# Kernel tuning notes

Measured on AMD Instinct MI355X. Metric: run time of the kernel, lower is better.

Reference implementation:

```python
import jax, jax.numpy as jnp
import numpy as np

B, T, D, U = 64, 2048, 512, 512

def setup_inputs() -> dict:
    key = jax.random.key(0)
    ks = jax.random.split(key, 5)
    scale = 1.0 / np.sqrt(D)
    return {
        "features": jax.random.normal(ks[0], (B, T, D), dtype=jnp.float32),
        "hidden": jax.random.normal(ks[1], (B, D), dtype=jnp.float32),
        "W1": jax.random.normal(ks[2], (D, U), dtype=jnp.float32) * scale,
        "b1": jnp.zeros((U,), dtype=jnp.float32),
        "W2": jax.random.normal(ks[3], (D, U), dtype=jnp.float32) * scale,
        "b2": jnp.zeros((U,), dtype=jnp.float32),
        "V": jax.random.normal(ks[4], (U, 1), dtype=jnp.float32) * (1.0 / np.sqrt(U)),
        "bV": jnp.zeros((1,), dtype=jnp.float32),
    }

def reference(features, hidden, W1, b1, W2, b2, V, bV):
    # features: [B, T, D]; hidden: [B, D]
    proj_f = jnp.einsum('btd,du->btu', features, W1) + b1          # [B, T, U]
    proj_h = (hidden @ W2 + b2)[:, None, :]                        # [B, 1, U]
    score = jnp.tanh(proj_f + proj_h) @ V + bV                     # [B, T, 1]
    attention_weights = jax.nn.softmax(score, axis=1)              # [B, T, 1]
    context_vector = jnp.sum(attention_weights * features, axis=1) # [B, D]
    return (context_vector, attention_weights)
```

## Files before the change

### kernel.cpp

```cpp
#include <hip/hip_runtime.h>
#include <hip/hip_bf16.h>

#define BB 64
#define TT 2048
#define DD 512
#define UU 512
#define MM (BB * TT)
#define CTX_ELEMS (BB * DD)
#define ATTN_OFF  CTX_ELEMS

typedef __bf16 bf16x8 __attribute__((ext_vector_type(8)));
typedef float  f32x4  __attribute__((ext_vector_type(4)));
typedef unsigned short u16x8 __attribute__((ext_vector_type(8)));
typedef unsigned int u32;

#define GLOBAL_AS __attribute__((address_space(1)))
#define LDS_AS    __attribute__((address_space(3)))

__device__ __forceinline__ unsigned short f2bf(float f) {
    union { float f; unsigned u; } x; x.f = f;
    unsigned r = x.u + 0x7fffu + ((x.u >> 16) & 1u);
    return (unsigned short)(r >> 16);
}

__device__ __forceinline__ float tanh_fast(float x) {
    x = fminf(fmaxf(x, -10.f), 10.f);
    float e = __builtin_amdgcn_exp2f(x * 2.885390082f);
    return (e - 1.0f) * __builtin_amdgcn_rcpf(e + 1.0f);
}

__global__ void k_w1t(const float* __restrict__ W1, unsigned short* __restrict__ W1T) {
    int gid = blockIdx.x * 256 + threadIdx.x;
    int u  = gid & 511;
    int dc = gid >> 9;
    int d0 = dc * 8;
    u16x8 pk;
    #pragma unroll
    for (int e = 0; e < 8; ++e)
        pk[e] = f2bf(W1[(size_t)(d0 + e) * UU + u]);
    int nt = u >> 7, n = u & 127;
    int kt = dc >> 2, kc = dc & 3;
    size_t off = ((size_t)(nt * 16 + kt) * 8192 + kc * 2048 + n * 16) / 2;
    *(u16x8*)(W1T + off) = pk;
}

__global__ void k_phc(const float* __restrict__ hidden, const float* __restrict__ W2,
                      const float* __restrict__ b1, const float* __restrict__ b2,
                      float* __restrict__ phc) {
    const int b = blockIdx.x;
    const int u = threadIdx.x;
    const float* h = hidden + (size_t)b * DD;
    float acc = b1[u] + b2[u];
    #pragma unroll 8
    for (int d = 0; d < DD; ++d)
        acc += h[d] * W2[(size_t)d * UU + u];
    phc[(size_t)b * UU + u] = acc;
}

__launch_bounds__(256, 3)
__global__ void k_score(const float* __restrict__ feat,
                        const unsigned short* __restrict__ W1T,
                        const float* __restrict__ phc,
                        const float* __restrict__ V,
                        float* __restrict__ part) {
    __shared__ float sA[128 * 32];
    __shared__ unsigned short sB[4096];
    __shared__ float sRed[4][64];

    const int tid  = threadIdx.x;
    const int lane = tid & 63;
    const int w    = tid >> 6;
    const int wr   = w >> 1, wc = w & 1;

    const int rb  = blockIdx.x;
    const int xcd = rb & 7;
    const int uu  = rb >> 3;
    const int gy  = uu & 3;
    const int gx  = xcd * 128 + (uu >> 2);
    const int m0  = gx * 128;
    const int b   = m0 >> 11;

    f32x4 acc[4][4];
    #pragma unroll
    for (int i = 0; i < 4; ++i)
        #pragma unroll
        for (int j = 0; j < 4; ++j)
            acc[i][j] = (f32x4){0.f, 0.f, 0.f, 0.f};

    const char* fbase0 = (const char*)feat + (size_t)m0 * 2048;
    const char* bslab0 = (const char*)W1T + (size_t)gy * 16 * 8192;

    for (int kt = 0; kt < 16; ++kt) {
        const char* bslab = bslab0 + kt * 8192;
        #pragma unroll
        for (int p = 0; p < 2; ++p) {
            int s = p * 256 + tid;
            const char* src = bslab + s * 16;
            char* dst = (char*)sB + (size_t)(p * 256 + (tid & ~63)) * 16;
            __builtin_amdgcn_global_load_lds((const GLOBAL_AS u32*)src, (LDS_AS u32*)dst, 16, 0, 0);
        }
        const char* fbase = fbase0 + kt * 128;
        #pragma unroll
        for (int j = 0; j < 4; ++j) {
            int s = j * 256 + tid;
            int row = s >> 3;
            int cpos = s & 7;
            int c = cpos ^ (row & 7);
            const char* src = fbase + (size_t)row * 2048 + c * 16;
            char* dst = (char*)sA + (size_t)(j * 256 + (tid & ~63)) * 16;
            __builtin_amdgcn_global_load_lds((const GLOBAL_AS u32*)src, (LDS_AS u32*)dst, 16, 0, 0);
        }
        __syncthreads();

        const int kc = lane >> 4;
        bf16x8 bfr[4];
        #pragma unroll
        for (int ns = 0; ns < 4; ++ns) {
            int n = wc * 64 + ns * 16 + (lane & 15);
            bfr[ns] = *(const bf16x8*)((const char*)sB + kc * 2048 + n * 16);
        }
        #pragma unroll
        for (int ms = 0; ms < 4; ++ms) {
            int m = wr * 64 + ms * 16 + (lane & 15);
            int c0 = (2 * kc) ^ (m & 7);
            int c1 = (2 * kc + 1) ^ (m & 7);
            f32x4 a0 = *(const f32x4*)((const char*)sA + m * 128 + c0 * 16);
            f32x4 a1 = *(const f32x4*)((const char*)sA + m * 128 + c1 * 16);
            bf16x8 af;
            #pragma unroll
            for (int j = 0; j < 4; ++j) { af[j] = (__bf16)a0[j]; af[4 + j] = (__bf16)a1[j]; }
            #pragma unroll
            for (int ns = 0; ns < 4; ++ns)
                acc[ms][ns] = __builtin_amdgcn_mfma_f32_16x16x32_bf16(af, bfr[ns], acc[ms][ns], 0, 0, 0);
        }
        __syncthreads();
    }

    float pc[4], vv[4];
    #pragma unroll
    for (int ns = 0; ns < 4; ++ns) {
        int ug = gy * 128 + wc * 64 + ns * 16 + (lane & 15);
        pc[ns] = phc[(size_t)b * UU + ug];
        vv[ns] = V[ug];
    }
    float pr[4][4];
    #pragma unroll
    for (int ms = 0; ms < 4; ++ms)
        #pragma unroll
        for (int rg = 0; rg < 4; ++rg) {
            float s = 0.f;
            #pragma unroll
            for (int ns = 0; ns < 4; ++ns)
                s += tanh_fast(acc[ms][ns][rg] + pc[ns]) * vv[ns];
            pr[ms][rg] = s;
        }
    #pragma unroll
    for (int off = 1; off < 16; off <<= 1)
        #pragma unroll
        for (int ms = 0; ms < 4; ++ms)
            #pragma unroll
            for (int rg = 0; rg < 4; ++rg)
                pr[ms][rg] += __shfl_xor(pr[ms][rg], off, 64);
    if ((lane & 15) == 0) {
        int rowg = lane >> 4;
        #pragma unroll
        for (int ms = 0; ms < 4; ++ms)
            #pragma unroll
            for (int rg = 0; rg < 4; ++rg)
                sRed[w][ms * 16 + rowg * 4 + rg] = pr[ms][rg];
    }
    __syncthreads();
    if (tid < 128) {
        int wrx = tid >> 6, ml = tid & 63;
        float v = sRed[2 * wrx][ml] + sRed[2 * wrx + 1][ml];
        part[(size_t)gy * MM + m0 + tid] = v;
    }
}

__global__ void k_softmax(const float* __restrict__ part, float* __restrict__ dout) {
    const int b = blockIdx.x, tid = threadIdx.x;
    float* sc = dout + ATTN_OFF + (size_t)b * TT;
    float v[8];
    float mx = -3.4e38f;
    #pragma unroll
    for (int i = 0; i < 8; ++i) {
        int t = tid + 256 * i;
        size_t idx = (size_t)b * TT + t;
        v[i] = part[idx] + part[MM + idx] + part[2 * MM + idx] + part[3 * MM + idx];
        mx = fmaxf(mx, v[i]);
    }
    __shared__ float red[256];
    red[tid] = mx; __syncthreads();
    for (int s = 128; s >= 1; s >>= 1) {
        if (tid < s) red[tid] = fmaxf(red[tid], red[tid + s]);
        __syncthreads();
    }
    mx = red[0]; __syncthreads();
    float sum = 0.f;
    #pragma unroll
    for (int i = 0; i < 8; ++i) { v[i] = __expf(v[i] - mx); sum += v[i]; }
    red[tid] = sum; __syncthreads();
    for (int s = 128; s >= 1; s >>= 1) {
        if (tid < s) red[tid] += red[tid + s];
        __syncthreads();
    }
    float inv = 1.0f / red[0];
    #pragma unroll
    for (int i = 0; i < 8; ++i) sc[tid + 256 * i] = v[i] * inv;
}

__global__ void k_context(const float* __restrict__ feat, float* __restrict__ dout) {
    const int b = blockIdx.x, dc = blockIdx.y;
    const int dq = threadIdx.x & 15;
    const int ty = threadIdx.x >> 4;
    const int d = dc * 64 + dq * 4;
    const float* wgt = dout + ATTN_OFF + (size_t)b * TT;
    const float* f = feat + (size_t)b * TT * DD + d;
    float4 acc = {0.f, 0.f, 0.f, 0.f};
    #pragma unroll 4
    for (int i = 0; i < TT / 16; ++i) {
        int t = i * 16 + ty;
        float wv = wgt[t];
        float4 fv = *(const float4*)(f + (size_t)t * DD);
        acc.x += wv * fv.x; acc.y += wv * fv.y;
        acc.z += wv * fv.z; acc.w += wv * fv.w;
    }
    __shared__ float4 red[16][16];
    red[ty][dq] = acc; __syncthreads();
    if (ty == 0) {
        float4 s = red[0][dq];
        #pragma unroll
        for (int k = 1; k < 16; ++k) {
            float4 r = red[k][dq];
            s.x += r.x; s.y += r.y; s.z += r.z; s.w += r.w;
        }
        *(float4*)(dout + (size_t)b * DD + d) = s;
    }
}

extern "C" void kernel_launch(void* const* d_in, const int* in_sizes, int n_in,
                              void* d_out, int out_size, void* d_ws, size_t ws_size,
                              hipStream_t stream) {
    (void)in_sizes; (void)n_in; (void)out_size; (void)ws_size;
    const float* feat   = (const float*)d_in[0];
    const float* hidden = (const float*)d_in[1];
    const float* W1     = (const float*)d_in[2];
    const float* b1     = (const float*)d_in[3];
    const float* W2     = (const float*)d_in[4];
    const float* b2     = (const float*)d_in[5];
    const float* V      = (const float*)d_in[6];

    unsigned short* W1T = (unsigned short*)d_ws;
    float* phc  = (float*)((char*)d_ws + 512 * 1024);
    float* part = (float*)((char*)d_ws + 640 * 1024);
    float* out  = (float*)d_out;

    hipLaunchKernelGGL(k_w1t,     dim3(128),    dim3(256), 0, stream, W1, W1T);
    hipLaunchKernelGGL(k_phc,     dim3(64),     dim3(512), 0, stream, hidden, W2, b1, b2, phc);
    hipLaunchKernelGGL(k_score,   dim3(4096),   dim3(256), 0, stream, feat, W1T, phc, V, part);
    hipLaunchKernelGGL(k_softmax, dim3(64),     dim3(256), 0, stream, part, out);
    hipLaunchKernelGGL(k_context, dim3(64, 8),  dim3(256), 0, stream, feat, out);
}
```

Measured before the change: 196.0 us.

## Double-buffer score GEMM with register-staged bf16 A tiles and larger blocks

Rewrites the score GEMM kernel to use 512-thread blocks that each cover 256 rows, with a K tile of 64 and double-buffered LDS for both operands. The next tile's feature loads and W1 loads are issued while the current tile's MFMAs run. Features are converted to bf16 once in registers before being written to LDS, instead of being stored as fp32 and converted by every wave on read. This is meant to hide global-memory latency and halve LDS traffic for A. The cost is higher register and LDS use per block and hand-written waitcnt/barrier scheduling that is fragile.

```diff
diff --git a/kernel.cpp b/kernel.cpp
--- a/kernel.cpp
+++ b/kernel.cpp
@@ -38,9 +38,9 @@
     #pragma unroll
     for (int e = 0; e < 8; ++e)
         pk[e] = f2bf(W1[(size_t)(d0 + e) * UU + u]);
-    int nt = u >> 7, n = u & 127;
-    int kt = dc >> 2, kc = dc & 3;
-    size_t off = ((size_t)(nt * 16 + kt) * 8192 + kc * 2048 + n * 16) / 2;
+    int gy = u >> 7, n = u & 127;
+    int kt = dc >> 3, kc = dc & 7;
+    size_t off = (((size_t)(gy * 8 + kt) * 8 + kc) * 1024 + n * 8);
     *(u16x8*)(W1T + off) = pk;
 }
 
@@ -57,29 +57,45 @@
     phc[(size_t)b * UU + u] = acc;
 }
 
-__launch_bounds__(256, 3)
+__launch_bounds__(512, 1)
 __global__ void k_score(const float* __restrict__ feat,
                         const unsigned short* __restrict__ W1T,
                         const float* __restrict__ phc,
                         const float* __restrict__ V,
                         float* __restrict__ part) {
-    __shared__ float sA[128 * 32];
-    __shared__ unsigned short sB[4096];
-    __shared__ float sRed[4][64];
+    __shared__ __align__(16) unsigned short sA[2 * 8 * 256 * 8];
+    __shared__ __align__(16) unsigned short sB[2 * 8 * 128 * 8];
+    __shared__ float sRed[8][64];
 
     const int tid  = threadIdx.x;
     const int lane = tid & 63;
     const int w    = tid >> 6;
-    const int wr   = w >> 1, wc = w & 1;
-
-    const int rb  = blockIdx.x;
-    const int xcd = rb & 7;
-    const int uu  = rb >> 3;
-    const int gy  = uu & 3;
-    const int gx  = xcd * 128 + (uu >> 2);
-    const int m0  = gx * 128;
+    const int wm   = w >> 1, wc = w & 1;
+
+    const int bid = blockIdx.x;
+    const int xcd = bid & 7;
+    const int idx = bid >> 3;
+    const int gy  = idx & 3;
+    const int mt  = xcd * 64 + (idx >> 2);
+    const int m0  = mt * 256;
     const int b   = m0 >> 11;
 
+    const int kcl   = lane >> 4;
+    const int rlane = lane & 15;
+
+    const char* fsrc = (const char*)feat +
+        (((size_t)(m0 + (tid >> 3)) * 512) + (size_t)(tid & 7) * 8) * 4;
+    const char* bsl = (const char*)W1T + (size_t)gy * 8 * 16384;
+
+    float pc[4], vv[4];
+    #pragma unroll
+    for (int ns = 0; ns < 4; ++ns) {
+        int ug = gy * 128 + wc * 64 + ns * 16 + rlane;
+        pc[ns] = phc[(size_t)b * UU + ug];
+        vv[ns] = V[ug];
+    }
+
+    f32x4 rA[8];
     f32x4 acc[4][4];
     #pragma unroll
     for (int i = 0; i < 4; ++i)
@@ -87,62 +103,92 @@
         for (int j = 0; j < 4; ++j)
             acc[i][j] = (f32x4){0.f, 0.f, 0.f, 0.f};
 
-    const char* fbase0 = (const char*)feat + (size_t)m0 * 2048;
-    const char* bslab0 = (const char*)W1T + (size_t)gy * 16 * 8192;
-
-    for (int kt = 0; kt < 16; ++kt) {
-        const char* bslab = bslab0 + kt * 8192;
-        #pragma unroll
-        for (int p = 0; p < 2; ++p) {
-            int s = p * 256 + tid;
-            const char* src = bslab + s * 16;
-            char* dst = (char*)sB + (size_t)(p * 256 + (tid & ~63)) * 16;
-            __builtin_amdgcn_global_load_lds((const GLOBAL_AS u32*)src, (LDS_AS u32*)dst, 16, 0, 0);
-        }
-        const char* fbase = fbase0 + kt * 128;
-        #pragma unroll
-        for (int j = 0; j < 4; ++j) {
-            int s = j * 256 + tid;
-            int row = s >> 3;
-            int cpos = s & 7;
-            int c = cpos ^ (row & 7);
-            const char* src = fbase + (size_t)row * 2048 + c * 16;
-            char* dst = (char*)sA + (size_t)(j * 256 + (tid & ~63)) * 16;
-            __builtin_amdgcn_global_load_lds((const GLOBAL_AS u32*)src, (LDS_AS u32*)dst, 16, 0, 0);
-        }
-        __syncthreads();
-
-        const int kc = lane >> 4;
-        bf16x8 bfr[4];
-        #pragma unroll
-        for (int ns = 0; ns < 4; ++ns) {
-            int n = wc * 64 + ns * 16 + (lane & 15);
-            bfr[ns] = *(const bf16x8*)((const char*)sB + kc * 2048 + n * 16);
-        }
-        #pragma unroll
-        for (int ms = 0; ms < 4; ++ms) {
-            int m = wr * 64 + ms * 16 + (lane & 15);
-            int c0 = (2 * kc) ^ (m & 7);
-            int c1 = (2 * kc + 1) ^ (m & 7);
-            f32x4 a0 = *(const f32x4*)((const char*)sA + m * 128 + c0 * 16);
-            f32x4 a1 = *(const f32x4*)((const char*)sA + m * 128 + c1 * 16);
-            bf16x8 af;
-            #pragma unroll
-            for (int j = 0; j < 4; ++j) { af[j] = (__bf16)a0[j]; af[4 + j] = (__bf16)a1[j]; }
-            #pragma unroll
-            for (int ns = 0; ns < 4; ++ns)
-                acc[ms][ns] = __builtin_amdgcn_mfma_f32_16x16x32_bf16(af, bfr[ns], acc[ms][ns], 0, 0, 0);
-        }
-        __syncthreads();
-    }
-
-    float pc[4], vv[4];
-    #pragma unroll
-    for (int ns = 0; ns < 4; ++ns) {
-        int ug = gy * 128 + wc * 64 + ns * 16 + (lane & 15);
-        pc[ns] = phc[(size_t)b * UU + ug];
-        vv[ns] = V[ug];
-    }
+#define VMW(N)  asm volatile("s_waitcnt vmcnt(" #N ")" ::: "memory")
+#define LGKM0() asm volatile("s_waitcnt lgkmcnt(0)" ::: "memory")
+
+#define ISSUE_A(tt_, p_) do {                                                    \
+    rA[4*(p_)+0] = *(const f32x4*)(fsrc + (size_t)(2*(p_))  *131072 + (tt_)*256);     \
+    rA[4*(p_)+1] = *(const f32x4*)(fsrc + (size_t)(2*(p_))  *131072 + (tt_)*256 + 16);\
+    rA[4*(p_)+2] = *(const f32x4*)(fsrc + (size_t)(2*(p_)+1)*131072 + (tt_)*256);     \
+    rA[4*(p_)+3] = *(const f32x4*)(fsrc + (size_t)(2*(p_)+1)*131072 + (tt_)*256 + 16);\
+    } while (0)
+
+#define ISSUE_B(tt_, p_) do {                                                    \
+    const char* src_ = bsl + (size_t)(tt_) * 16384 + (p_) * 8192 + tid * 16;     \
+    char* dst_ = (char*)sB + ((tt_) & 1) * 16384 + (p_) * 8192 + (tid & ~63) * 16;\
+    __builtin_amdgcn_global_load_lds((const GLOBAL_AS u32*)src_,                 \
+                                     (LDS_AS u32*)dst_, 16, 0, 0); } while (0)
+
+#define WRITE_A(tt_) do {                                                        \
+    const int kcw_ = tid & 7;                                                    \
+    _Pragma("unroll")                                                            \
+    for (int j_ = 0; j_ < 4; ++j_) {                                             \
+        bf16x8 q_;                                                               \
+        _Pragma("unroll")                                                        \
+        for (int e_ = 0; e_ < 4; ++e_) {                                         \
+            q_[e_]     = (__bf16)rA[2*j_][e_];                                   \
+            q_[4 + e_] = (__bf16)rA[2*j_ + 1][e_];                               \
+        }                                                                        \
+        int row_ = j_ * 64 + (tid >> 3);                                         \
+        int byt_ = ((tt_) & 1) * 32768 + kcw_ * 4096 + ((row_ * 16) ^ (kcw_ * 16));\
+        *(bf16x8*)((char*)sA + byt_) = q_;                                       \
+    } } while (0)
+
+#define PH(t_, p_, PRE_, VM_) do {                                               \
+    bf16x8 af[4], bfr[4];                                                        \
+    _Pragma("unroll")                                                            \
+    for (int ms_ = 0; ms_ < 4; ++ms_) {                                          \
+        int kc_ = (p_) * 4 + kcl;                                                \
+        int row_ = wm * 64 + ms_ * 16 + rlane;                                   \
+        af[ms_] = *(const bf16x8*)((const char*)sA + ((t_) & 1) * 32768 +        \
+                   kc_ * 4096 + ((row_ * 16) ^ (kc_ * 16)));                     \
+    }                                                                            \
+    _Pragma("unroll")                                                            \
+    for (int ns_ = 0; ns_ < 4; ++ns_) {                                          \
+        int kc_ = (p_) * 4 + kcl;                                                \
+        bfr[ns_] = *(const bf16x8*)((const char*)sB + ((t_) & 1) * 16384 +       \
+                    kc_ * 2048 + (wc * 64 + ns_ * 16 + rlane) * 16);             \
+    }                                                                            \
+    if (PRE_) { ISSUE_A((t_) + 1, p_); ISSUE_B((t_) + 1, p_); }                  \
+    if ((VM_) == 0) VMW(5); else if ((VM_) == 1) VMW(1); else if ((VM_) == 2) VMW(0); \
+    if ((p_) == 1 && (PRE_)) WRITE_A((t_) + 1);                                  \
+    LGKM0();                                                                     \
+    __builtin_amdgcn_s_barrier();                                                \
+    __builtin_amdgcn_sched_barrier(0);                                           \
+    __builtin_amdgcn_s_setprio(1);                                               \
+    _Pragma("unroll")                                                            \
+    for (int ms_ = 0; ms_ < 4; ++ms_)                                            \
+        _Pragma("unroll")                                                        \
+        for (int ns_ = 0; ns_ < 4; ++ns_)                                        \
+            acc[ms_][ns_] = __builtin_amdgcn_mfma_f32_16x16x32_bf16(             \
+                af[ms_], bfr[ns_], acc[ms_][ns_], 0, 0, 0);                      \
+    __builtin_amdgcn_s_setprio(0); } while (0)
+
+    ISSUE_A(0, 0);
+    ISSUE_A(0, 1);
+    ISSUE_B(0, 0);
+    ISSUE_B(0, 1);
+    VMW(1);
+    WRITE_A(0);
+    LGKM0();
+    __builtin_amdgcn_s_barrier();
+
+    PH(0, 0, 1, 0); PH(0, 1, 1, 1);
+    PH(1, 0, 1, 0); PH(1, 1, 1, 1);
+    PH(2, 0, 1, 0); PH(2, 1, 1, 1);
+    PH(3, 0, 1, 0); PH(3, 1, 1, 1);
+    PH(4, 0, 1, 0); PH(4, 1, 1, 1);
+    PH(5, 0, 1, 0); PH(5, 1, 1, 1);
+    PH(6, 0, 1, 0); PH(6, 1, 1, 1);
+    PH(7, 0, 0, 2); PH(7, 1, 0, 3);
+
+#undef PH
+#undef WRITE_A
+#undef ISSUE_B
+#undef ISSUE_A
+#undef VMW
+#undef LGKM0
+
     float pr[4][4];
     #pragma unroll
     for (int ms = 0; ms < 4; ++ms)
@@ -161,6 +207,7 @@
             #pragma unroll
             for (int rg = 0; rg < 4; ++rg)
                 pr[ms][rg] += __shfl_xor(pr[ms][rg], off, 64);
+    __syncthreads();
     if ((lane & 15) == 0) {
         int rowg = lane >> 4;
         #pragma unroll
@@ -170,9 +217,9 @@
                 sRed[w][ms * 16 + rowg * 4 + rg] = pr[ms][rg];
     }
     __syncthreads();
-    if (tid < 128) {
-        int wrx = tid >> 6, ml = tid & 63;
-        float v = sRed[2 * wrx][ml] + sRed[2 * wrx + 1][ml];
+    if (tid < 256) {
+        int wmx = tid >> 6, r = tid & 63;
+        float v = sRed[2 * wmx][r] + sRed[2 * wmx + 1][r];
         part[(size_t)gy * MM + m0 + tid] = v;
     }
 }
@@ -257,7 +304,7 @@
 
     hipLaunchKernelGGL(k_w1t,     dim3(128),    dim3(256), 0, stream, W1, W1T);
     hipLaunchKernelGGL(k_phc,     dim3(64),     dim3(512), 0, stream, hidden, W2, b1, b2, phc);
-    hipLaunchKernelGGL(k_score,   dim3(4096),   dim3(256), 0, stream, feat, W1T, phc, V, part);
+    hipLaunchKernelGGL(k_score,   dim3(2048),   dim3(512), 0, stream, feat, W1T, phc, V, part);
     hipLaunchKernelGGL(k_softmax, dim3(64),     dim3(256), 0, stream, part, out);
     hipLaunchKernelGGL(k_context, dim3(64, 8),  dim3(256), 0, stream, feat, out);
 }
```

Result: slower. 225.9 us (+15.3%).

## Pipeline score GEMM with register-staged bf16 A tile and double-buffered B

Applied to the files above, without the earlier changes.

The score kernel's main loop now uses K-steps of 64 instead of 32 (8 iterations). The next feature tile is prefetched into registers and the next W1 tile goes into a second LDS buffer while MFMAs run on the current one. Features are converted to bf16 once when stored to LDS, with an XOR swizzle, instead of being re-converted from fp32 LDS by each wave. The W1 pre-transpose layout changes to match. This aims to hide global-load latency and cut LDS traffic and conversion work, at the cost of more registers and hand-placed waitcnt/barrier ordering that could limit occupancy or be fragile.

```diff
diff --git a/kernel.cpp b/kernel.cpp
--- a/kernel.cpp
+++ b/kernel.cpp
@@ -38,10 +38,11 @@
     #pragma unroll
     for (int e = 0; e < 8; ++e)
         pk[e] = f2bf(W1[(size_t)(d0 + e) * UU + u]);
-    int nt = u >> 7, n = u & 127;
-    int kt = dc >> 2, kc = dc & 3;
-    size_t off = ((size_t)(nt * 16 + kt) * 8192 + kc * 2048 + n * 16) / 2;
-    *(u16x8*)(W1T + off) = pk;
+    int gy = u >> 7, n = u & 127;
+    int kt = dc >> 3, kc8 = dc & 7;
+    size_t off = (size_t)gy * 131072 + (size_t)kt * 16384 + kc8 * 2048
+               + ((n * 16) ^ (kc8 << 4));
+    *(u16x8*)((char*)W1T + off) = pk;
 }
 
 __global__ void k_phc(const float* __restrict__ hidden, const float* __restrict__ W2,
@@ -63,14 +64,15 @@
                         const float* __restrict__ phc,
                         const float* __restrict__ V,
                         float* __restrict__ part) {
-    __shared__ float sA[128 * 32];
-    __shared__ unsigned short sB[4096];
+    __shared__ __align__(16) unsigned short sA[8 * 128 * 8];
+    __shared__ __align__(16) unsigned short sB[2][8 * 128 * 8];
     __shared__ float sRed[4][64];
 
-    const int tid  = threadIdx.x;
-    const int lane = tid & 63;
-    const int w    = tid >> 6;
-    const int wr   = w >> 1, wc = w & 1;
+    const int tid   = threadIdx.x;
+    const int lane  = tid & 63;
+    const int w     = tid >> 6;
+    const int wm    = w >> 1, wc = w & 1;
+    const int rlane = lane & 15;
 
     const int rb  = blockIdx.x;
     const int xcd = rb & 7;
@@ -80,6 +82,22 @@
     const int m0  = gx * 128;
     const int b   = m0 >> 11;
 
+    const char* bsl = (const char*)W1T + (size_t)gy * 131072;
+
+    const int row_s = tid >> 1;
+    const int h_s   = tid & 1;
+    const char* fA = (const char*)feat +
+        ((size_t)(m0 + row_s) * 512 + (size_t)h_s * 32) * 4;
+
+    float pc[4], vv[4];
+    #pragma unroll
+    for (int ns = 0; ns < 4; ++ns) {
+        int ug = gy * 128 + wc * 64 + ns * 16 + rlane;
+        pc[ns] = phc[(size_t)b * UU + ug];
+        vv[ns] = V[ug];
+    }
+
+    f32x4 rS[8];
     f32x4 acc[4][4];
     #pragma unroll
     for (int i = 0; i < 4; ++i)
@@ -87,62 +105,85 @@
         for (int j = 0; j < 4; ++j)
             acc[i][j] = (f32x4){0.f, 0.f, 0.f, 0.f};
 
-    const char* fbase0 = (const char*)feat + (size_t)m0 * 2048;
-    const char* bslab0 = (const char*)W1T + (size_t)gy * 16 * 8192;
-
-    for (int kt = 0; kt < 16; ++kt) {
-        const char* bslab = bslab0 + kt * 8192;
-        #pragma unroll
-        for (int p = 0; p < 2; ++p) {
-            int s = p * 256 + tid;
-            const char* src = bslab + s * 16;
-            char* dst = (char*)sB + (size_t)(p * 256 + (tid & ~63)) * 16;
-            __builtin_amdgcn_global_load_lds((const GLOBAL_AS u32*)src, (LDS_AS u32*)dst, 16, 0, 0);
-        }
-        const char* fbase = fbase0 + kt * 128;
-        #pragma unroll
-        for (int j = 0; j < 4; ++j) {
-            int s = j * 256 + tid;
-            int row = s >> 3;
-            int cpos = s & 7;
-            int c = cpos ^ (row & 7);
-            const char* src = fbase + (size_t)row * 2048 + c * 16;
-            char* dst = (char*)sA + (size_t)(j * 256 + (tid & ~63)) * 16;
-            __builtin_amdgcn_global_load_lds((const GLOBAL_AS u32*)src, (LDS_AS u32*)dst, 16, 0, 0);
-        }
-        __syncthreads();
-
-        const int kc = lane >> 4;
-        bf16x8 bfr[4];
-        #pragma unroll
-        for (int ns = 0; ns < 4; ++ns) {
-            int n = wc * 64 + ns * 16 + (lane & 15);
-            bfr[ns] = *(const bf16x8*)((const char*)sB + kc * 2048 + n * 16);
-        }
-        #pragma unroll
-        for (int ms = 0; ms < 4; ++ms) {
-            int m = wr * 64 + ms * 16 + (lane & 15);
-            int c0 = (2 * kc) ^ (m & 7);
-            int c1 = (2 * kc + 1) ^ (m & 7);
-            f32x4 a0 = *(const f32x4*)((const char*)sA + m * 128 + c0 * 16);
-            f32x4 a1 = *(const f32x4*)((const char*)sA + m * 128 + c1 * 16);
-            bf16x8 af;
-            #pragma unroll
-            for (int j = 0; j < 4; ++j) { af[j] = (__bf16)a0[j]; af[4 + j] = (__bf16)a1[j]; }
-            #pragma unroll
-            for (int ns = 0; ns < 4; ++ns)
-                acc[ms][ns] = __builtin_amdgcn_mfma_f32_16x16x32_bf16(af, bfr[ns], acc[ms][ns], 0, 0, 0);
-        }
-        __syncthreads();
-    }
-
-    float pc[4], vv[4];
-    #pragma unroll
-    for (int ns = 0; ns < 4; ++ns) {
-        int ug = gy * 128 + wc * 64 + ns * 16 + (lane & 15);
-        pc[ns] = phc[(size_t)b * UU + ug];
-        vv[ns] = V[ug];
-    }
+#define ISSUE_A(kt_) do {                                                     \
+    _Pragma("unroll")                                                         \
+    for (int q_ = 0; q_ < 8; ++q_)                                            \
+        rS[q_] = *(const f32x4*)(fA + (kt_) * 256 + q_ * 16); } while (0)
+
+#define ISSUE_B(kt_) do {                                                     \
+    _Pragma("unroll")                                                         \
+    for (int p_ = 0; p_ < 4; ++p_) {                                          \
+        const char* src_ = bsl + (size_t)(kt_) * 16384 + p_ * 4096 + tid * 16;\
+        char* dst_ = (char*)&sB[(kt_) & 1][0] + p_ * 4096 + (tid & ~63) * 16; \
+        __builtin_amdgcn_global_load_lds((const GLOBAL_AS u32*)src_,          \
+                                         (LDS_AS u32*)dst_, 16, 0, 0);        \
+    } } while (0)
+
+#define WRITE_A() do {                                                        \
+    _Pragma("unroll")                                                         \
+    for (int j_ = 0; j_ < 4; ++j_) {                                          \
+        bf16x8 q_;                                                            \
+        _Pragma("unroll")                                                     \
+        for (int e_ = 0; e_ < 4; ++e_) {                                      \
+            q_[e_]     = (__bf16)rS[2 * j_][e_];                              \
+            q_[4 + e_] = (__bf16)rS[2 * j_ + 1][e_];                          \
+        }                                                                     \
+        int kc8_ = 4 * h_s + j_;                                              \
+        *(bf16x8*)((char*)sA + kc8_ * 2048 + ((row_s * 16) ^ (kc8_ << 4))) = q_; \
+    } } while (0)
+
+#define DO_C(c_, cb_) do {                                                    \
+    const int kc8_ = (c_) * 4 + (lane >> 4);                                  \
+    const int xr_  = kc8_ << 4;                                               \
+    bf16x8 af_[4], bf_[4];                                                    \
+    _Pragma("unroll")                                                         \
+    for (int ms_ = 0; ms_ < 4; ++ms_)                                         \
+        af_[ms_] = *(const bf16x8*)((const char*)sA + kc8_ * 2048 +           \
+                   (((wm * 64 + ms_ * 16 + rlane) * 16) ^ xr_));              \
+    _Pragma("unroll")                                                         \
+    for (int ns_ = 0; ns_ < 4; ++ns_)                                         \
+        bf_[ns_] = *(const bf16x8*)((const char*)&sB[cb_][0] + kc8_ * 2048 +  \
+                   (((wc * 64 + ns_ * 16 + rlane) * 16) ^ xr_));              \
+    _Pragma("unroll")                                                         \
+    for (int ms_ = 0; ms_ < 4; ++ms_)                                         \
+        _Pragma("unroll")                                                     \
+        for (int ns_ = 0; ns_ < 4; ++ns_)                                     \
+            acc[ms_][ns_] = __builtin_amdgcn_mfma_f32_16x16x32_bf16(          \
+                af_[ms_], bf_[ns_], acc[ms_][ns_], 0, 0, 0); } while (0)
+
+#define STEP(kt_) do {                                                        \
+    if ((kt_) < 7) {                                                          \
+        ISSUE_A((kt_) + 1); ISSUE_B((kt_) + 1);                               \
+        __builtin_amdgcn_sched_barrier(0);                                    \
+    }                                                                         \
+    DO_C(0, (kt_) & 1); DO_C(1, (kt_) & 1);                                   \
+    asm volatile("s_waitcnt lgkmcnt(0)" ::: "memory");                        \
+    __builtin_amdgcn_s_barrier();                                             \
+    if ((kt_) < 7) {                                                          \
+        asm volatile("s_waitcnt vmcnt(4)" ::: "memory");                      \
+        WRITE_A();                                                            \
+        asm volatile("s_waitcnt vmcnt(0)" ::: "memory");                      \
+        asm volatile("s_waitcnt lgkmcnt(0)" ::: "memory");                    \
+        __builtin_amdgcn_s_barrier();                                         \
+    } } while (0)
+
+    ISSUE_A(0); ISSUE_B(0);
+    __builtin_amdgcn_sched_barrier(0);
+    asm volatile("s_waitcnt vmcnt(4)" ::: "memory");
+    WRITE_A();
+    asm volatile("s_waitcnt vmcnt(0)" ::: "memory");
+    asm volatile("s_waitcnt lgkmcnt(0)" ::: "memory");
+    __builtin_amdgcn_s_barrier();
+
+    STEP(0); STEP(1); STEP(2); STEP(3);
+    STEP(4); STEP(5); STEP(6); STEP(7);
+
+#undef STEP
+#undef DO_C
+#undef WRITE_A
+#undef ISSUE_B
+#undef ISSUE_A
+
     float pr[4][4];
     #pragma unroll
     for (int ms = 0; ms < 4; ++ms)
```

Measured after the change: 283.7 us. 1.45x slower.

## Pipeline score GEMM with triple-buffered A and double-buffered B LDS rings

Applied to the files above, without the earlier changes.

Replaces the single-buffered load/sync/compute loop in the score GEMM with a fully unrolled software pipeline. Feature tiles go into a 3-stage LDS ring and W1 tiles into a 2-stage ring, synchronised with explicit vmcnt waits and one barrier per k-step instead of two. The W1T layout gets an XOR swizzle to cut LDS bank conflicts, and MFMA sections run at raised wave priority. The larger LDS footprint lowers the occupancy target from 3 to 2 blocks per CU, so the change relies on overlap rather than more resident waves to hide memory latency.

```diff
diff --git a/kernel.cpp b/kernel.cpp
--- a/kernel.cpp
+++ b/kernel.cpp
@@ -38,10 +38,11 @@
     #pragma unroll
     for (int e = 0; e < 8; ++e)
         pk[e] = f2bf(W1[(size_t)(d0 + e) * UU + u]);
-    int nt = u >> 7, n = u & 127;
-    int kt = dc >> 2, kc = dc & 3;
-    size_t off = ((size_t)(nt * 16 + kt) * 8192 + kc * 2048 + n * 16) / 2;
-    *(u16x8*)(W1T + off) = pk;
+    int gy = u >> 7, n = u & 127;
+    int kt32 = dc >> 2, kc = dc & 3;
+    size_t off = (size_t)gy * 131072 + (size_t)kt32 * 8192 + kc * 2048
+               + ((n * 16) ^ (kc << 4));
+    *(u16x8*)((char*)W1T + off) = pk;
 }
 
 __global__ void k_phc(const float* __restrict__ hidden, const float* __restrict__ W2,
@@ -57,20 +58,22 @@
     phc[(size_t)b * UU + u] = acc;
 }
 
-__launch_bounds__(256, 3)
+__launch_bounds__(256, 2)
 __global__ void k_score(const float* __restrict__ feat,
                         const unsigned short* __restrict__ W1T,
                         const float* __restrict__ phc,
                         const float* __restrict__ V,
                         float* __restrict__ part) {
-    __shared__ float sA[128 * 32];
-    __shared__ unsigned short sB[4096];
+    __shared__ __align__(16) char ringA[3][16384];
+    __shared__ __align__(16) char ringB[2][8192];
     __shared__ float sRed[4][64];
 
-    const int tid  = threadIdx.x;
-    const int lane = tid & 63;
-    const int w    = tid >> 6;
-    const int wr   = w >> 1, wc = w & 1;
+    const int tid   = threadIdx.x;
+    const int lane  = tid & 63;
+    const int w     = tid >> 6;
+    const int wm    = w >> 1, wc = w & 1;
+    const int rl    = lane & 15;
+    const int kcl   = lane >> 4;
 
     const int rb  = blockIdx.x;
     const int xcd = rb & 7;
@@ -80,6 +83,12 @@
     const int m0  = gx * 128;
     const int b   = m0 >> 11;
 
+    const char* fb  = (const char*)feat + (size_t)m0 * 2048;
+    const char* bsl = (const char*)W1T + (size_t)gy * 131072;
+
+    const int arow = tid >> 3;
+    const int axor = (((tid & 7) ^ ((tid >> 3) & 7)) << 4);
+
     f32x4 acc[4][4];
     #pragma unroll
     for (int i = 0; i < 4; ++i)
@@ -87,59 +96,88 @@
         for (int j = 0; j < 4; ++j)
             acc[i][j] = (f32x4){0.f, 0.f, 0.f, 0.f};
 
-    const char* fbase0 = (const char*)feat + (size_t)m0 * 2048;
-    const char* bslab0 = (const char*)W1T + (size_t)gy * 16 * 8192;
-
-    for (int kt = 0; kt < 16; ++kt) {
-        const char* bslab = bslab0 + kt * 8192;
-        #pragma unroll
-        for (int p = 0; p < 2; ++p) {
-            int s = p * 256 + tid;
-            const char* src = bslab + s * 16;
-            char* dst = (char*)sB + (size_t)(p * 256 + (tid & ~63)) * 16;
-            __builtin_amdgcn_global_load_lds((const GLOBAL_AS u32*)src, (LDS_AS u32*)dst, 16, 0, 0);
-        }
-        const char* fbase = fbase0 + kt * 128;
-        #pragma unroll
-        for (int j = 0; j < 4; ++j) {
-            int s = j * 256 + tid;
-            int row = s >> 3;
-            int cpos = s & 7;
-            int c = cpos ^ (row & 7);
-            const char* src = fbase + (size_t)row * 2048 + c * 16;
-            char* dst = (char*)sA + (size_t)(j * 256 + (tid & ~63)) * 16;
-            __builtin_amdgcn_global_load_lds((const GLOBAL_AS u32*)src, (LDS_AS u32*)dst, 16, 0, 0);
-        }
-        __syncthreads();
-
-        const int kc = lane >> 4;
-        bf16x8 bfr[4];
-        #pragma unroll
-        for (int ns = 0; ns < 4; ++ns) {
-            int n = wc * 64 + ns * 16 + (lane & 15);
-            bfr[ns] = *(const bf16x8*)((const char*)sB + kc * 2048 + n * 16);
-        }
-        #pragma unroll
-        for (int ms = 0; ms < 4; ++ms) {
-            int m = wr * 64 + ms * 16 + (lane & 15);
-            int c0 = (2 * kc) ^ (m & 7);
-            int c1 = (2 * kc + 1) ^ (m & 7);
-            f32x4 a0 = *(const f32x4*)((const char*)sA + m * 128 + c0 * 16);
-            f32x4 a1 = *(const f32x4*)((const char*)sA + m * 128 + c1 * 16);
-            bf16x8 af;
-            #pragma unroll
-            for (int j = 0; j < 4; ++j) { af[j] = (__bf16)a0[j]; af[4 + j] = (__bf16)a1[j]; }
-            #pragma unroll
-            for (int ns = 0; ns < 4; ++ns)
-                acc[ms][ns] = __builtin_amdgcn_mfma_f32_16x16x32_bf16(af, bfr[ns], acc[ms][ns], 0, 0, 0);
-        }
-        __syncthreads();
-    }
+#define VMW(N)  asm volatile("s_waitcnt vmcnt(" #N ")" ::: "memory")
+
+#define ISSUE_A(kt_, s_) do {                                                  \
+    _Pragma("unroll")                                                          \
+    for (int p_ = 0; p_ < 4; ++p_) {                                           \
+        const char* src_ = fb + (size_t)(p_ * 32 + arow) * 2048 +              \
+                           (kt_) * 128 + axor;                                 \
+        char* dst_ = (char*)&ringA[s_][0] + p_ * 4096 + (tid & ~63) * 16;      \
+        __builtin_amdgcn_global_load_lds((const GLOBAL_AS u32*)src_,           \
+                                         (LDS_AS u32*)dst_, 16, 0, 0);         \
+    } } while (0)
+
+#define ISSUE_B(kt_, s_) do {                                                  \
+    _Pragma("unroll")                                                          \
+    for (int p_ = 0; p_ < 2; ++p_) {                                           \
+        const char* src_ = bsl + (size_t)(kt_) * 8192 + p_ * 4096 + tid * 16;  \
+        char* dst_ = (char*)&ringB[s_][0] + p_ * 4096 + (tid & ~63) * 16;      \
+        __builtin_amdgcn_global_load_lds((const GLOBAL_AS u32*)src_,           \
+                                         (LDS_AS u32*)dst_, 16, 0, 0);         \
+    } } while (0)
+
+#define COMPUTE(kt_) do {                                                      \
+    const char* aS_ = &ringA[(kt_) % 3][0];                                    \
+    const char* bS_ = &ringB[(kt_) & 1][0];                                    \
+    bf16x8 af_[4], bf_[4];                                                     \
+    _Pragma("unroll")                                                          \
+    for (int ms_ = 0; ms_ < 4; ++ms_) {                                        \
+        int row_ = wm * 64 + ms_ * 16 + rl;                                    \
+        int off_ = row_ * 128 + ((kcl * 32) ^ ((row_ & 7) << 4));              \
+        f32x4 lo_ = *(const f32x4*)(aS_ + off_);                               \
+        f32x4 hi_ = *(const f32x4*)(aS_ + (off_ ^ 16));                        \
+        _Pragma("unroll")                                                      \
+        for (int j_ = 0; j_ < 4; ++j_) {                                       \
+            af_[ms_][j_]     = (__bf16)lo_[j_];                                \
+            af_[ms_][4 + j_] = (__bf16)hi_[j_];                                \
+        }                                                                      \
+    }                                                                          \
+    _Pragma("unroll")                                                          \
+    for (int ns_ = 0; ns_ < 4; ++ns_) {                                        \
+        int n_ = wc * 64 + ns_ * 16 + rl;                                      \
+        bf_[ns_] = *(const bf16x8*)(bS_ + kcl * 2048 +                         \
+                                    ((n_ * 16) ^ (kcl << 4)));                 \
+    }                                                                          \
+    __builtin_amdgcn_s_setprio(1);                                             \
+    _Pragma("unroll")                                                          \
+    for (int ms_ = 0; ms_ < 4; ++ms_)                                          \
+        _Pragma("unroll")                                                      \
+        for (int ns_ = 0; ns_ < 4; ++ns_)                                      \
+            acc[ms_][ns_] = __builtin_amdgcn_mfma_f32_16x16x32_bf16(           \
+                af_[ms_], bf_[ns_], acc[ms_][ns_], 0, 0, 0);                   \
+    __builtin_amdgcn_s_setprio(0); } while (0)
+
+#define EPOCH(kt_, IB_, IA_, NW_) do {                                         \
+    VMW(NW_);                                                                  \
+    __builtin_amdgcn_s_barrier();                                              \
+    __builtin_amdgcn_sched_barrier(0);                                         \
+    if (IB_) ISSUE_B((kt_) + 1, ((kt_) + 1) & 1);                              \
+    if (IA_) ISSUE_A((kt_) + 2, ((kt_) + 2) % 3);                              \
+    COMPUTE(kt_); } while (0)
+
+    ISSUE_A(0, 0);
+    ISSUE_B(0, 0);
+    ISSUE_A(1, 1);
+
+    EPOCH(0,  1, 1, 4);  EPOCH(1,  1, 1, 4);  EPOCH(2,  1, 1, 4);
+    EPOCH(3,  1, 1, 4);  EPOCH(4,  1, 1, 4);  EPOCH(5,  1, 1, 4);
+    EPOCH(6,  1, 1, 4);  EPOCH(7,  1, 1, 4);  EPOCH(8,  1, 1, 4);
+    EPOCH(9,  1, 1, 4);  EPOCH(10, 1, 1, 4);  EPOCH(11, 1, 1, 4);
+    EPOCH(12, 1, 1, 4);  EPOCH(13, 1, 1, 4);
+    EPOCH(14, 1, 0, 4);
+    EPOCH(15, 0, 0, 0);
+
+#undef EPOCH
+#undef COMPUTE
+#undef ISSUE_B
+#undef ISSUE_A
+#undef VMW
 
     float pc[4], vv[4];
     #pragma unroll
     for (int ns = 0; ns < 4; ++ns) {
-        int ug = gy * 128 + wc * 64 + ns * 16 + (lane & 15);
+        int ug = gy * 128 + wc * 64 + ns * 16 + rl;
         pc[ns] = phc[(size_t)b * UU + ug];
         vv[ns] = V[ug];
     }
```

Result: slower. 216.4 us (+10.4%).
